# Kernel tuning notes

Hardware: AMD Instinct MI355X
Metric: run time of the kernel (lower is better)

## Reference

```python
import jax, jax.numpy as jnp
import numpy as np

DEPTH = 4  # 2**DEPTH - 1 = 15 decision nodes, 2**DEPTH = 16 leaves


def setup_inputs() -> dict:
    key = jax.random.key(0)
    k1, k2, k3, k4, k5 = jax.random.split(key, 5)
    B, S, H = 2, 2048, 1024
    n_dec, n_leaf = 2 ** DEPTH - 1, 2 ** DEPTH
    s = 1.0 / np.sqrt(H)
    return {
        "x": jax.random.normal(k1, (B, S, H), dtype=jnp.float32),
        "Wd": jax.random.normal(k2, (n_dec, H, 2), dtype=jnp.float32) * s,
        "bd": jax.random.normal(k3, (n_dec, 2), dtype=jnp.float32) * s,
        "Wl": jax.random.normal(k4, (n_leaf, H, H), dtype=jnp.float32) * s,
        "bl": jax.random.normal(k5, (n_leaf, H), dtype=jnp.float32) * s,
    }


def reference(x, Wd, bd, Wl, bl):
    B, S, H = x.shape
    # All decision nodes in one grouped GEMM: [B,S,n_dec,2], independent sigmoids
    decisions = jax.nn.sigmoid(jnp.einsum('bsh,nhk->bsnk', x, Wd) + bd)
    # Cumulative path probabilities with torch-faithful cat([p*left, p*right]) ordering
    path = jnp.ones((B, S, 1), dtype=x.dtype)
    for level in range(DEPTH):
        start = 2 ** level - 1
        lv = decisions[:, :, start:start + 2 ** level, :]  # [B,S,2^level,2]
        path = jnp.concatenate([path * lv[..., 0], path * lv[..., 1]], axis=-1)
    # Weighted leaf-output sum without materializing [B,S,n_leaf,H]
    out = jnp.einsum('bsh,lhd,bsl->bsd', x, Wl, path, optimize=True)
    out = out + jnp.einsum('bsl,ld->bsd', path, bl)
    return out
```

## Files before the change

### kernel.cpp

```cpp
#include <hip/hip_runtime.h>
#include <hip/hip_bf16.h>

typedef unsigned short u16;
typedef unsigned int u32;
typedef short bf16x8 __attribute__((ext_vector_type(8)));
typedef _Float16 f16x8 __attribute__((ext_vector_type(8)));
typedef float f32x4 __attribute__((ext_vector_type(4)));

__device__ __forceinline__ u16 f2bf(float f) {
    u32 u = __builtin_bit_cast(u32, f);
    u32 r = (u + 0x7FFFu + ((u >> 16) & 1u)) >> 16;
    return (u16)r;
}
__device__ __forceinline__ u16 f2h(float f) {
    _Float16 h = (_Float16)f;
    return __builtin_bit_cast(u16, h);
}

__device__ __forceinline__ void lds16(const void* g, void* s) {
    __builtin_amdgcn_global_load_lds(
        (const __attribute__((address_space(1))) u32*)g,
        (__attribute__((address_space(3))) u32*)s, 16, 0, 0);
}

__global__ __launch_bounds__(256) void pre_kernel(
    const float* __restrict__ x, const float* __restrict__ Wd,
    const float* __restrict__ bd, const float* __restrict__ Wl,
    float* __restrict__ path, u16* __restrict__ xb, u16* __restrict__ wlt,
    int as_f16, int M) {
    __shared__ float tile[64][65];
    const int bid = blockIdx.x;

    if (bid < 4096) {
        int nb = bid & 15, hb = (bid >> 4) & 15, l = bid >> 8;
        int t = threadIdx.x;
        int r = t >> 2, cq = (t & 3) << 4;

        const float* src = Wl + ((size_t)(l * 1024 + hb * 64 + r)) * 1024 + nb * 64 + cq;
#pragma unroll
        for (int j = 0; j < 4; ++j) {
            float4 w = ((const float4*)src)[j];
            tile[r][cq + 4 * j + 0] = w.x;
            tile[r][cq + 4 * j + 1] = w.y;
            tile[r][cq + 4 * j + 2] = w.z;
            tile[r][cq + 4 * j + 3] = w.w;
        }
        __syncthreads();
        union { u16 u[16]; uint4 q[2]; } pk;
#pragma unroll
        for (int j = 0; j < 16; ++j)
            pk.u[j] = as_f16 ? f2h(tile[cq + j][r]) : f2bf(tile[cq + j][r]);
        u16* dst = wlt + ((size_t)(l * 1024 + nb * 64 + r)) * 1024 + hb * 64 + cq;
        ((uint4*)dst)[0] = pk.q[0];
        ((uint4*)dst)[1] = pk.q[1];
        return;
    }

    int lane = threadIdx.x & 63;
    int wid = threadIdx.x >> 6;
    int m = (bid - 4096) * 4 + wid;
    if (m >= M) return;

    const float* xr = x + (size_t)m * 1024;
    float v[16];
#pragma unroll
    for (int i = 0; i < 16; ++i) v[i] = xr[lane + 64 * i];
#pragma unroll
    for (int i = 0; i < 16; ++i)
        xb[(size_t)m * 1024 + lane + 64 * i] = as_f16 ? f2h(v[i]) : f2bf(v[i]);

    int leaf = lane & 15;
    int nd[4], bit[4];
#pragma unroll
    for (int k = 0; k < 4; ++k) {
        nd[k] = (1 << k) - 1 + (leaf & ((1 << k) - 1));
        bit[k] = (leaf >> k) & 1;
    }
    float z[4] = {0.f, 0.f, 0.f, 0.f};

    const float2* Wd2 = (const float2*)Wd;
    for (int n = 0; n < 15; ++n) {
        float s0 = 0.f, s1 = 0.f;
#pragma unroll
        for (int i = 0; i < 16; ++i) {
            float2 w = Wd2[n * 1024 + lane + 64 * i];
            s0 += v[i] * w.x;
            s1 += v[i] * w.y;
        }
#pragma unroll
        for (int off = 32; off; off >>= 1) {
            s0 += __shfl_xor(s0, off, 64);
            s1 += __shfl_xor(s1, off, 64);
        }
#pragma unroll
        for (int k = 0; k < 4; ++k)
            if (nd[k] == n) z[k] = bit[k] ? s1 : s0;
    }
    float p = 1.f;
#pragma unroll
    for (int k = 0; k < 4; ++k) {
        float zz = z[k] + bd[nd[k] * 2 + bit[k]];
        p *= 1.f / (1.f + expf(-zz));
    }
    if (lane < 16) path[(size_t)m * 16 + leaf] = p;
}

__global__ __launch_bounds__(512, 2) void tree_gemm8(
    const u16* __restrict__ xh, const u16* __restrict__ wlt,
    const float* __restrict__ path, float* __restrict__ out,
    float* __restrict__ part, int M) {
    __shared__ __align__(16) u16 Asm[2][2][128 * 64];
    __shared__ __align__(16) u16 Bsm[2][2][128 * 64];
    __shared__ u16 psm_h[4][256];

    const int tid = threadIdx.x, lane = tid & 63, w = tid >> 6;
    const int wm = w >> 2, wn = w & 3;
    const int nbm = M >> 8;
    int xb_, yb_, zb_;
    {
        int bid = blockIdx.x;
        if ((nbm << 4) == 256) {
            int k = bid & 7, s = bid >> 3;
            zb_ = k >> 1; yb_ = (k & 1) * 8 + (s >> 2); xb_ = s & 3;
        } else {
            xb_ = bid & 3; int t2 = bid >> 2; yb_ = t2 % nbm; zb_ = t2 / nbm;
        }
    }
    const int n0 = xb_ * 256, m0 = yb_ * 256, z = zb_;
    const int z4 = z * 4;
    const int rl = lane >> 3;
    const int srcswz = ((lane & 7) ^ rl) << 4;
    const int arow = (lane & 15) * 128;
    const int coff0 = ((lane >> 4) << 4) ^ ((lane & 7) << 4);

    for (int i = tid; i < 1024; i += 512) {
        int r = i >> 2, lz = i & 3;
        psm_h[lz][r] = f2h(path[(size_t)(m0 + r) * 16 + z4 + lz]);
    }

#define ISSUE_A_H(dst_, ks_, h_)                                                    \
    {                                                                               \
        _Pragma("unroll") for (int j_ = 0; j_ < 2; ++j_)                            \
            lds16((const char*)xh +                                                 \
                      (size_t)(m0 + (h_) * 128 + w * 16 + j_ * 8 + rl) * 2048 +     \
                      ((ks_) << 7) + srcswz,                                        \
                  (dst_) + (h_) * 16384 + w * 2048 + j_ * 1024);                    \
    }
#define ISSUE_A(dst_, ks_) { ISSUE_A_H(dst_, ks_, 0); ISSUE_A_H(dst_, ks_, 1); }
#define ISSUE_B(dst_, t_)                                                           \
    if ((t_) < 64) {                                                                \
        size_t lb_ = (size_t)(z4 + ((t_) & 3)) * 2097152 +                          \
                     ((size_t)((t_) >> 2) << 7);                                    \
        _Pragma("unroll") for (int h_ = 0; h_ < 2; ++h_)                            \
        _Pragma("unroll") for (int j_ = 0; j_ < 2; ++j_)                            \
            lds16((const char*)wlt + lb_ +                                          \
                      (size_t)(n0 + h_ * 128 + w * 16 + j_ * 8 + rl) * 2048 +       \
                      srcswz,                                                       \
                  (dst_) + h_ * 16384 + w * 2048 + j_ * 1024);                      \
    }
#define LDA4(aB_, mfb)                                                              \
    _Pragma("unroll") for (int q_ = 0; q_ < 4; ++q_) {                              \
        aR[q_][0] = *(const f16x8*)((aB_) + ((mfb) + q_) * 2048 + coff0);           \
        aR[q_][1] = *(const f16x8*)((aB_) + ((mfb) + q_) * 2048 + (coff0 ^ 64));    \
    }
#define LDB2(bB_, nfb, d0)                                                          \
    _Pragma("unroll") for (int q_ = 0; q_ < 2; ++q_) {                              \
        bR[(d0) + q_][0] = *(const f16x8*)((bB_) + ((nfb) + q_) * 2048 + coff0);    \
        bR[(d0) + q_][1] =                                                          \
            *(const f16x8*)((bB_) + ((nfb) + q_) * 2048 + (coff0 ^ 64));            \
    }
#define LDP(ll, mfb)                                                                \
    _Pragma("unroll") for (int q_ = 0; q_ < 4; ++q_)                                \
        p2[q_] = __builtin_bit_cast(                                                \
            _Float16, psm_h[ll][wm * 128 + ((mfb) + q_) * 16 + (lane & 15)]);
#define SCALE                                                                       \
    _Pragma("unroll") for (int q_ = 0; q_ < 4; ++q_) {                              \
        aR[q_][0] *= p2[q_];                                                        \
        aR[q_][1] *= p2[q_];                                                        \
    }
#define MM(a0, b0)                                                                  \
    _Pragma("unroll") for (int mq_ = 0; mq_ < 4; ++mq_)                             \
    _Pragma("unroll") for (int nq_ = 0; nq_ < 2; ++nq_) {                           \
        acc[(a0) + mq_][(b0) + nq_] = __builtin_amdgcn_mfma_f32_16x16x32_f16(       \
            aR[mq_][0], bR[(b0) + nq_][0], acc[(a0) + mq_][(b0) + nq_], 0, 0, 0);   \
        acc[(a0) + mq_][(b0) + nq_] = __builtin_amdgcn_mfma_f32_16x16x32_f16(       \
            aR[mq_][1], bR[(b0) + nq_][1], acc[(a0) + mq_][(b0) + nq_], 0, 0, 0);   \
    }
#define BAR __builtin_amdgcn_s_barrier()
#define LG0 asm volatile("s_waitcnt lgkmcnt(0)" ::: "memory")
#define PRIO1 __builtin_amdgcn_s_setprio(1)
#define PRIO0 __builtin_amdgcn_s_setprio(0)
#define VM0 asm volatile("s_waitcnt vmcnt(0)" ::: "memory")
#define VM8 asm volatile("s_waitcnt vmcnt(8)" ::: "memory")
#define VM16 asm volatile("s_waitcnt vmcnt(16)" ::: "memory")
#define NOPX ((void)0)

#define TILE(aB_, bB_, ll, EB2, EA0, EA1, WT)                                       \
    {                                                                               \
        f16x8 aR[4][2], bR[4][2];                                                   \
        _Float16 p2[4];                                                             \
                                                                      \
        LDA4(aB_, 0); LDB2(bB_, 0, 0); LDP(ll, 0);                                  \
        BAR; LG0; SCALE; PRIO1; MM(0, 0); PRIO0; BAR;                               \
                                                                      \
        LDB2(bB_, 2, 2);                                                            \
        BAR; LG0; PRIO1; MM(0, 2); PRIO0; BAR;                                      \
                  \
        LDA4(aB_, 4); LDP(ll, 4); EB2; EA0;                                         \
        BAR; LG0; SCALE; PRIO1; MM(4, 0); PRIO0; BAR;                               \
                      \
        EA1;                                                                        \
        PRIO1; MM(4, 2); PRIO0; WT; BAR;                                            \
    }

    f32x4 acc[8][4];
#pragma unroll
    for (int a = 0; a < 8; ++a)
#pragma unroll
        for (int b = 0; b < 4; ++b) acc[a][b] = (f32x4){0.f, 0.f, 0.f, 0.f};

    const char* aBase0 = (const char*)Asm[0][wm] + arow;
    const char* aBase1 = (const char*)Asm[1][wm] + arow;
    const char* bBase0 = (const char*)Bsm[0][wn >> 1] + (wn & 1) * 8192 + arow;
    const char* bBase1 = (const char*)Bsm[1][wn >> 1] + (wn & 1) * 8192 + arow;
    char* aSlot0 = (char*)Asm[0][0];
    char* aSlot1 = (char*)Asm[1][0];
    char* bSlot0 = (char*)Bsm[0][0];
    char* bSlot1 = (char*)Bsm[1][0];

    ISSUE_A(aSlot0, 0);
    ISSUE_B(bSlot0, 0);
    ISSUE_B(bSlot1, 1);
    asm volatile("s_waitcnt vmcnt(8) lgkmcnt(0)" ::: "memory");
    BAR;
    __builtin_amdgcn_sched_barrier(0);

#pragma unroll 1
    for (int ks = 0; ks < 15; ++ks) {
        const int t4 = ks << 2;
        const char* aB = (ks & 1) ? aBase1 : aBase0;
        char* aD = (ks & 1) ? aSlot0 : aSlot1;
        TILE(aB, bBase0, 0, ISSUE_B(bSlot0, t4 + 2), NOPX, NOPX, VM8);
        TILE(aB, bBase1, 1, ISSUE_B(bSlot1, t4 + 3),
             ISSUE_A_H(aD, ks + 1, 0), ISSUE_A_H(aD, ks + 1, 1), VM16);
        TILE(aB, bBase0, 2, ISSUE_B(bSlot0, t4 + 4), NOPX, NOPX, VM16);
        TILE(aB, bBase1, 3, ISSUE_B(bSlot1, t4 + 5), NOPX, NOPX, VM8);
    }
    {
        const char* aB = aBase1;
        TILE(aB, bBase0, 0, ISSUE_B(bSlot0, 62), NOPX, NOPX, VM8);
        TILE(aB, bBase1, 1, ISSUE_B(bSlot1, 63), NOPX, NOPX, VM8);
        TILE(aB, bBase0, 2, NOPX, NOPX, NOPX, VM0);
        TILE(aB, bBase1, 3, NOPX, NOPX, NOPX, NOPX);
    }

    float* po = (z == 0) ? out : part + (size_t)(z - 1) * M * 1024;
    const int r0 = m0 + wm * 128 + ((lane >> 4) << 2);
    const int c0 = n0 + wn * 64 + (lane & 15);
#pragma unroll
    for (int mf = 0; mf < 8; ++mf)
#pragma unroll
        for (int jj = 0; jj < 4; ++jj)
#pragma unroll
            for (int nf = 0; nf < 4; ++nf)
                po[(size_t)(r0 + mf * 16 + jj) * 1024 + c0 + nf * 16] = acc[mf][nf][jj];
#undef ISSUE_A_H
#undef ISSUE_A
#undef ISSUE_B
#undef LDA4
#undef LDB2
#undef LDP
#undef SCALE
#undef MM
#undef BAR
#undef LG0
#undef PRIO1
#undef PRIO0
#undef VM0
#undef VM8
#undef VM16
#undef NOPX
#undef TILE
}

__global__ __launch_bounds__(256) void tree_gemm_fb(
    const u16* __restrict__ xb, const u16* __restrict__ wlt,
    const float* __restrict__ path, float* __restrict__ pout,
    int M, int LPB, int lgLPB) {
    __shared__ __align__(16) u16 Asm[128 * 64];
    __shared__ __align__(16) u16 Bsm[128 * 64];
    __shared__ float psm[128][16];

    const int tid = threadIdx.x, lane = tid & 63, wid = tid >> 6;
    const int wm = wid >> 1, wn = wid & 1;
    const int m0 = blockIdx.y * 128, n0 = blockIdx.x * 128;
    const int lbase = blockIdx.z * LPB;

    for (int i = tid; i < (128 << lgLPB); i += 256) {
        int r = i >> lgLPB, c = i & (LPB - 1);
        psm[r][c] = path[(size_t)(m0 + r) * 16 + lbase + c];
    }

    const int colb = (((lane & 7) ^ (lane >> 3)) << 4);
    const int rl = lane >> 3;

    f32x4 accF[4][4], accL[4][4];
#pragma unroll
    for (int a = 0; a < 4; ++a)
#pragma unroll
        for (int b = 0; b < 4; ++b) {
            accF[a][b] = (f32x4){0.f, 0.f, 0.f, 0.f};
            accL[a][b] = (f32x4){0.f, 0.f, 0.f, 0.f};
        }

    const int nsteps = LPB << 4;
    for (int sl = 0; sl < nsteps; ++sl) {
        const int l_ = lbase + (sl >> 4);
        const int h2_ = (sl & 15) << 7;
#pragma unroll
        for (int i_ = 0; i_ < 4; ++i_) {
            int seg_ = wid * 4 + i_;
            int r_ = seg_ * 8 + rl;
            lds16((const char*)xb + (size_t)(m0 + r_) * 2048 + h2_ + colb,
                  (char*)Asm + seg_ * 1024);
            lds16((const char*)wlt + (size_t)(l_ * 1024 + n0 + r_) * 2048 + h2_ + colb,
                  (char*)Bsm + seg_ * 1024);
        }
        __syncthreads();

#pragma unroll
        for (int kf = 0; kf < 2; ++kf) {
            int c2 = kf * 64 + ((lane >> 4) << 4);
            bf16x8 af[4], bfr[4];
#pragma unroll
            for (int mf = 0; mf < 4; ++mf) {
                int rr = wm * 64 + mf * 16 + (lane & 15);
                af[mf] = *(const bf16x8*)((const char*)Asm + rr * 128 + (c2 ^ ((lane & 7) << 4)));
            }
#pragma unroll
            for (int nf = 0; nf < 4; ++nf) {
                int rr = wn * 64 + nf * 16 + (lane & 15);
                bfr[nf] = *(const bf16x8*)((const char*)Bsm + rr * 128 + (c2 ^ ((lane & 7) << 4)));
            }
#pragma unroll
            for (int mf = 0; mf < 4; ++mf)
#pragma unroll
                for (int nf = 0; nf < 4; ++nf)
                    accL[mf][nf] = __builtin_amdgcn_mfma_f32_16x16x32_bf16(
                        af[mf], bfr[nf], accL[mf][nf], 0, 0, 0);
        }
        __syncthreads();

        if ((sl & 15) == 15) {
            int ll = sl >> 4;
#pragma unroll
            for (int mf = 0; mf < 4; ++mf)
#pragma unroll
                for (int jj = 0; jj < 4; ++jj) {
                    float p = psm[wm * 64 + mf * 16 + ((lane >> 4) << 2) + jj][ll];
#pragma unroll
                    for (int nf = 0; nf < 4; ++nf) {
                        accF[mf][nf][jj] += p * accL[mf][nf][jj];
                        accL[mf][nf][jj] = 0.f;
                    }
                }
        }
    }

    float* po = pout + (size_t)blockIdx.z * M * 1024;
#pragma unroll
    for (int mf = 0; mf < 4; ++mf)
#pragma unroll
        for (int jj = 0; jj < 4; ++jj) {
            int rowl = wm * 64 + mf * 16 + ((lane >> 4) << 2) + jj;
#pragma unroll
            for (int nf = 0; nf < 4; ++nf) {
                int col = n0 + wn * 64 + nf * 16 + (lane & 15);
                po[(size_t)(m0 + rowl) * 1024 + col] = accF[mf][nf][jj];
            }
        }
}

__global__ __launch_bounds__(256) void reduce_kernel(
    const float* __restrict__ extra, const float* __restrict__ path,
    const float* __restrict__ bl, float* __restrict__ out, int M,
    int nExtra, int readOut) {
    int m = blockIdx.x, t = threadIdx.x;
    size_t i4 = (size_t)m * 256 + t;
    f32x4 acc = {0.f, 0.f, 0.f, 0.f};
    if (readOut) acc = ((const f32x4*)out)[i4];
    for (int g = 0; g < nExtra; ++g)
        acc += ((const f32x4*)extra)[(size_t)g * M * 256 + i4];
#pragma unroll
    for (int l = 0; l < 16; ++l) {
        float p = path[(size_t)m * 16 + l];
        f32x4 b = ((const f32x4*)bl)[l * 256 + t];
        acc += p * b;
    }
    ((f32x4*)out)[i4] = acc;
}

extern "C" void kernel_launch(void* const* d_in, const int* in_sizes, int n_in,
                              void* d_out, int out_size, void* d_ws, size_t ws_size,
                              hipStream_t stream) {
    const float* x  = (const float*)d_in[0];
    const float* Wd = (const float*)d_in[1];
    const float* bd = (const float*)d_in[2];
    const float* Wl = (const float*)d_in[3];
    const float* bl = (const float*)d_in[4];
    float* out = (float*)d_out;

    const int H = 1024;
    const int M = in_sizes[0] / H;
    char* ws = (char*)d_ws;

    size_t n_off_xh   = (size_t)M * 16 * 4;
    size_t n_off_wlt  = n_off_xh + (size_t)M * 1024 * 2;
    size_t n_off_part = n_off_wlt + (size_t)16 * 1024 * 1024 * 2;
    size_t n_need     = n_off_part + 3 * (size_t)M * 1024 * 4;

    if (ws_size >= n_need && (M % 256) == 0) {
        float* path = (float*)ws;
        u16* xh  = (u16*)(ws + n_off_xh);
        u16* wlt = (u16*)(ws + n_off_wlt);
        float* part = (float*)(ws + n_off_part);

        pre_kernel<<<4096 + M / 4, 256, 0, stream>>>(x, Wd, bd, Wl, path, xh, wlt, 1, M);
        tree_gemm8<<<4 * (M / 256) * 4, 512, 0, stream>>>(xh, wlt, path, out, part, M);
        reduce_kernel<<<M, 256, 0, stream>>>(part, path, bl, out, M, 3, 1);
        return;
    }

    size_t off_xb   = (size_t)M * 16 * 4;
    size_t off_wlt  = off_xb + (size_t)M * 1024 * 2;
    size_t off_part = off_wlt + (size_t)16 * 1024 * 1024 * 2;
    size_t per_part = (size_t)M * 1024 * 4;

    int G = 1;
    if (ws_size >= off_part + 4 * per_part) G = 4;
    else if (ws_size >= off_part + 2 * per_part) G = 2;
    const int LPB = 16 / G;
    const int lgLPB = (G == 1) ? 4 : (G == 2) ? 3 : 2;

    float* path = (float*)ws;
    u16* xb  = (u16*)(ws + off_xb);
    u16* wlt = (u16*)(ws + off_wlt);
    float* pout = (G == 1) ? out : (float*)(ws + off_part);

    pre_kernel<<<4096 + (M + 3) / 4, 256, 0, stream>>>(x, Wd, bd, Wl, path, xb, wlt, 0, M);
    tree_gemm_fb<<<dim3(8, M / 128, G), 256, 0, stream>>>(xb, wlt, path, pout, M, LPB, lgLPB);
    reduce_kernel<<<M, 256, 0, stream>>>(pout, path, bl, out, M,
                                         (G == 1) ? 0 : G, (G == 1) ? 1 : 0);
}
```

Before: 209.1 us.

## Hold A tile in registers across leaves and triple-buffer B in LDS

The kernel now loads the full 128-row A fragment for each k-step into registers once and reuses it for all four leaves, instead of re-reading A from LDS for every leaf. A uses a single LDS buffer that is refilled mid-iteration. B gets a rotating triple buffer so prefetch runs one stage further ahead. The path scaling is fused into the MFMA loop. This cuts LDS read traffic and barriers but raises VGPR pressure through the aU[8][2] array. The A refill also relies on the new wait counts being correct.

```diff
diff --git a/kernel.cpp b/kernel.cpp
--- a/kernel.cpp
+++ b/kernel.cpp
@@ -109,8 +109,8 @@
     const u16* __restrict__ xh, const u16* __restrict__ wlt,
     const float* __restrict__ path, float* __restrict__ out,
     float* __restrict__ part, int M) {
-    __shared__ __align__(16) u16 Asm[2][2][128 * 64];
-    __shared__ __align__(16) u16 Bsm[2][2][128 * 64];
+    __shared__ __align__(16) u16 Asm[2][128 * 64];
+    __shared__ __align__(16) u16 Bsm[3][2][128 * 64];
     __shared__ u16 psm_h[4][256];
 
     const int tid = threadIdx.x, lane = tid & 63, w = tid >> 6;
@@ -138,15 +138,14 @@
         psm_h[lz][r] = f2h(path[(size_t)(m0 + r) * 16 + z4 + lz]);
     }
 
-#define ISSUE_A_H(dst_, ks_, h_)                                                    \
+#define ISSUE_A_H(ks_, h_)                                                          \
     {                                                                               \
         _Pragma("unroll") for (int j_ = 0; j_ < 2; ++j_)                            \
             lds16((const char*)xh +                                                 \
                       (size_t)(m0 + (h_) * 128 + w * 16 + j_ * 8 + rl) * 2048 +     \
                       ((ks_) << 7) + srcswz,                                        \
-                  (dst_) + (h_) * 16384 + w * 2048 + j_ * 1024);                    \
-    }
-#define ISSUE_A(dst_, ks_) { ISSUE_A_H(dst_, ks_, 0); ISSUE_A_H(dst_, ks_, 1); }
+                  (char*)Asm[0] + (h_) * 16384 + w * 2048 + j_ * 1024);             \
+    }
 #define ISSUE_B(dst_, t_)                                                           \
     if ((t_) < 64) {                                                                \
         size_t lb_ = (size_t)(z4 + ((t_) & 3)) * 2097152 +                          \
@@ -158,59 +157,65 @@
                       srcswz,                                                       \
                   (dst_) + h_ * 16384 + w * 2048 + j_ * 1024);                      \
     }
-#define LDA4(aB_, mfb)                                                              \
-    _Pragma("unroll") for (int q_ = 0; q_ < 4; ++q_) {                              \
-        aR[q_][0] = *(const f16x8*)((aB_) + ((mfb) + q_) * 2048 + coff0);           \
-        aR[q_][1] = *(const f16x8*)((aB_) + ((mfb) + q_) * 2048 + (coff0 ^ 64));    \
-    }
-#define LDB2(bB_, nfb, d0)                                                          \
+#define LDA16                                                                       \
+    _Pragma("unroll") for (int r_ = 0; r_ < 8; ++r_) {                              \
+        aU[r_][0] = *(const f16x8*)(aRd + r_ * 2048 + coff0);                       \
+        aU[r_][1] = *(const f16x8*)(aRd + r_ * 2048 + (coff0 ^ 64));                \
+    }
+#define LDB2P(b0_)                                                                  \
     _Pragma("unroll") for (int q_ = 0; q_ < 2; ++q_) {                              \
-        bR[(d0) + q_][0] = *(const f16x8*)((bB_) + ((nfb) + q_) * 2048 + coff0);    \
-        bR[(d0) + q_][1] =                                                          \
-            *(const f16x8*)((bB_) + ((nfb) + q_) * 2048 + (coff0 ^ 64));            \
-    }
-#define LDP(ll, mfb)                                                                \
-    _Pragma("unroll") for (int q_ = 0; q_ < 4; ++q_)                                \
-        p2[q_] = __builtin_bit_cast(                                                \
-            _Float16, psm_h[ll][wm * 128 + ((mfb) + q_) * 16 + (lane & 15)]);
-#define SCALE                                                                       \
-    _Pragma("unroll") for (int q_ = 0; q_ < 4; ++q_) {                              \
-        aR[q_][0] *= p2[q_];                                                        \
-        aR[q_][1] *= p2[q_];                                                        \
-    }
-#define MM(a0, b0)                                                                  \
-    _Pragma("unroll") for (int mq_ = 0; mq_ < 4; ++mq_)                             \
-    _Pragma("unroll") for (int nq_ = 0; nq_ < 2; ++nq_) {                           \
-        acc[(a0) + mq_][(b0) + nq_] = __builtin_amdgcn_mfma_f32_16x16x32_f16(       \
-            aR[mq_][0], bR[(b0) + nq_][0], acc[(a0) + mq_][(b0) + nq_], 0, 0, 0);   \
-        acc[(a0) + mq_][(b0) + nq_] = __builtin_amdgcn_mfma_f32_16x16x32_f16(       \
-            aR[mq_][1], bR[(b0) + nq_][1], acc[(a0) + mq_][(b0) + nq_], 0, 0, 0);   \
+        bR[q_][0] = *(const f16x8*)(bRdA + ((b0_) + q_) * 2048 + coff0);            \
+        bR[q_][1] = *(const f16x8*)(bRdA + ((b0_) + q_) * 2048 + (coff0 ^ 64));     \
+    }
+#define LDP8(ll)                                                                    \
+    _Pragma("unroll") for (int r_ = 0; r_ < 8; ++r_)                                \
+        pc[r_] = __builtin_bit_cast(                                                \
+            _Float16, psm_h[ll][wm * 128 + r_ * 16 + (lane & 15)]);
+#define QMM(b0_)                                                                    \
+    _Pragma("unroll") for (int r_ = 0; r_ < 8; ++r_) {                              \
+        f16x8 s0_ = aU[r_][0] * pc[r_];                                             \
+        f16x8 s1_ = aU[r_][1] * pc[r_];                                             \
+        acc[r_][(b0_)] = __builtin_amdgcn_mfma_f32_16x16x32_f16(                    \
+            s0_, bR[0][0], acc[r_][(b0_)], 0, 0, 0);                                \
+        acc[r_][(b0_)] = __builtin_amdgcn_mfma_f32_16x16x32_f16(                    \
+            s1_, bR[0][1], acc[r_][(b0_)], 0, 0, 0);                                \
+        acc[r_][(b0_) + 1] = __builtin_amdgcn_mfma_f32_16x16x32_f16(                \
+            s0_, bR[1][0], acc[r_][(b0_) + 1], 0, 0, 0);                            \
+        acc[r_][(b0_) + 1] = __builtin_amdgcn_mfma_f32_16x16x32_f16(                \
+            s1_, bR[1][1], acc[r_][(b0_) + 1], 0, 0, 0);                            \
     }
 #define BAR __builtin_amdgcn_s_barrier()
 #define LG0 asm volatile("s_waitcnt lgkmcnt(0)" ::: "memory")
 #define PRIO1 __builtin_amdgcn_s_setprio(1)
 #define PRIO0 __builtin_amdgcn_s_setprio(0)
 #define VM0 asm volatile("s_waitcnt vmcnt(0)" ::: "memory")
-#define VM8 asm volatile("s_waitcnt vmcnt(8)" ::: "memory")
-#define VM16 asm volatile("s_waitcnt vmcnt(16)" ::: "memory")
+#define VM4 asm volatile("s_waitcnt vmcnt(4)" ::: "memory")
+#define VM12 asm volatile("s_waitcnt vmcnt(12)" ::: "memory")
 #define NOPX ((void)0)
-
-#define TILE(aB_, bB_, ll, EB2, EA0, EA1, WT)                                       \
+#define ROT                                                                         \
     {                                                                               \
-        f16x8 aR[4][2], bR[4][2];                                                   \
-        _Float16 p2[4];                                                             \
-                                                                      \
-        LDA4(aB_, 0); LDB2(bB_, 0, 0); LDP(ll, 0);                                  \
-        BAR; LG0; SCALE; PRIO1; MM(0, 0); PRIO0; BAR;                               \
-                                                                      \
-        LDB2(bB_, 2, 2);                                                            \
-        BAR; LG0; PRIO1; MM(0, 2); PRIO0; BAR;                                      \
-                  \
-        LDA4(aB_, 4); LDP(ll, 4); EB2; EA0;                                         \
-        BAR; LG0; SCALE; PRIO1; MM(4, 0); PRIO0; BAR;                               \
-                      \
+        const char* tr_ = bRdA; bRdA = bRdB; bRdB = bRdC; bRdC = tr_;               \
+        char* tw_ = bWrA; bWrA = bWrB; bWrB = bWrC; bWrC = tw_;                     \
+    }
+
+#define TILE(ll, LA, EB, EA0, EA1, WT)                                              \
+    {                                                                               \
+        f16x8 bR[2][2];                                                             \
+        _Float16 pc[8];                                                             \
+                                                                 \
+        EB; EA0;                                                                    \
+        LA;                                                                         \
+        LDB2P(0);                                                                   \
+        LDP8(ll);                                                                   \
+        BAR; LG0;                                                                   \
+        PRIO1; QMM(0); PRIO0;                                                       \
+        BAR;                                                                        \
+                                                                 \
+        LDB2P(2);                                                                   \
         EA1;                                                                        \
-        PRIO1; MM(4, 2); PRIO0; WT; BAR;                                            \
+        BAR; LG0;                                                                   \
+        PRIO1; QMM(2); PRIO0;                                                       \
+        WT; BAR;                                                                    \
     }
 
     f32x4 acc[8][4];
@@ -218,40 +223,38 @@
     for (int a = 0; a < 8; ++a)
 #pragma unroll
         for (int b = 0; b < 4; ++b) acc[a][b] = (f32x4){0.f, 0.f, 0.f, 0.f};
-
-    const char* aBase0 = (const char*)Asm[0][wm] + arow;
-    const char* aBase1 = (const char*)Asm[1][wm] + arow;
-    const char* bBase0 = (const char*)Bsm[0][wn >> 1] + (wn & 1) * 8192 + arow;
-    const char* bBase1 = (const char*)Bsm[1][wn >> 1] + (wn & 1) * 8192 + arow;
-    char* aSlot0 = (char*)Asm[0][0];
-    char* aSlot1 = (char*)Asm[1][0];
-    char* bSlot0 = (char*)Bsm[0][0];
-    char* bSlot1 = (char*)Bsm[1][0];
-
-    ISSUE_A(aSlot0, 0);
-    ISSUE_B(bSlot0, 0);
-    ISSUE_B(bSlot1, 1);
-    asm volatile("s_waitcnt vmcnt(8) lgkmcnt(0)" ::: "memory");
+    f16x8 aU[8][2];
+
+    const char* aRd = (const char*)Asm[wm] + arow;
+    const int bOff = (wn >> 1) * 16384 + (wn & 1) * 8192 + arow;
+    const char* bRdA = (const char*)Bsm[0][0] + bOff;
+    const char* bRdB = (const char*)Bsm[1][0] + bOff;
+    const char* bRdC = (const char*)Bsm[2][0] + bOff;
+    char* bWrA = (char*)Bsm[0][0];
+    char* bWrB = (char*)Bsm[1][0];
+    char* bWrC = (char*)Bsm[2][0];
+
+    ISSUE_A_H(0, 0); ISSUE_A_H(0, 1);
+    ISSUE_B(bWrA, 0);
+    ISSUE_B(bWrB, 1);
+    asm volatile("s_waitcnt vmcnt(4) lgkmcnt(0)" ::: "memory");
     BAR;
     __builtin_amdgcn_sched_barrier(0);
 
 #pragma unroll 1
     for (int ks = 0; ks < 15; ++ks) {
         const int t4 = ks << 2;
-        const char* aB = (ks & 1) ? aBase1 : aBase0;
-        char* aD = (ks & 1) ? aSlot0 : aSlot1;
-        TILE(aB, bBase0, 0, ISSUE_B(bSlot0, t4 + 2), NOPX, NOPX, VM8);
-        TILE(aB, bBase1, 1, ISSUE_B(bSlot1, t4 + 3),
-             ISSUE_A_H(aD, ks + 1, 0), ISSUE_A_H(aD, ks + 1, 1), VM16);
-        TILE(aB, bBase0, 2, ISSUE_B(bSlot0, t4 + 4), NOPX, NOPX, VM16);
-        TILE(aB, bBase1, 3, ISSUE_B(bSlot1, t4 + 5), NOPX, NOPX, VM8);
+        TILE(0, LDA16, ISSUE_B(bWrC, t4 + 2), NOPX, NOPX, VM4); ROT;
+        TILE(1, NOPX, ISSUE_B(bWrC, t4 + 3), NOPX, NOPX, VM4); ROT;
+        TILE(2, NOPX, ISSUE_B(bWrC, t4 + 4),
+             ISSUE_A_H(ks + 1, 0), ISSUE_A_H(ks + 1, 1), VM12); ROT;
+        TILE(3, NOPX, ISSUE_B(bWrC, t4 + 5), NOPX, NOPX, VM4); ROT;
     }
     {
-        const char* aB = aBase1;
-        TILE(aB, bBase0, 0, ISSUE_B(bSlot0, 62), NOPX, NOPX, VM8);
-        TILE(aB, bBase1, 1, ISSUE_B(bSlot1, 63), NOPX, NOPX, VM8);
-        TILE(aB, bBase0, 2, NOPX, NOPX, NOPX, VM0);
-        TILE(aB, bBase1, 3, NOPX, NOPX, NOPX, NOPX);
+        TILE(0, LDA16, ISSUE_B(bWrC, 62), NOPX, NOPX, VM4); ROT;
+        TILE(1, NOPX, ISSUE_B(bWrC, 63), NOPX, NOPX, VM4); ROT;
+        TILE(2, NOPX, NOPX, NOPX, NOPX, VM0); ROT;
+        TILE(3, NOPX, NOPX, NOPX, NOPX, NOPX);
     }
 
     float* po = (z == 0) ? out : part + (size_t)(z - 1) * M * 1024;
@@ -265,21 +268,20 @@
             for (int nf = 0; nf < 4; ++nf)
                 po[(size_t)(r0 + mf * 16 + jj) * 1024 + c0 + nf * 16] = acc[mf][nf][jj];
 #undef ISSUE_A_H
-#undef ISSUE_A
 #undef ISSUE_B
-#undef LDA4
-#undef LDB2
-#undef LDP
-#undef SCALE
-#undef MM
+#undef LDA16
+#undef LDB2P
+#undef LDP8
+#undef QMM
 #undef BAR
 #undef LG0
 #undef PRIO1
 #undef PRIO0
 #undef VM0
-#undef VM8
-#undef VM16
+#undef VM4
+#undef VM12
 #undef NOPX
+#undef ROT
 #undef TILE
 }
 
```

Measured after the change: 546.6 us. 2.61x slower.

## Split prologue into path and weight-transpose kernels; merge MFMA phases per tile

Applied to the files above, without the earlier changes.

The combined preprocessing kernel becomes two launches: one computes path probabilities and converts x, the other transposes and converts Wl. Inside the main GEMM each tile now loads both B halves together and runs MFMA in two larger phases instead of four, which removes two barrier pairs per tile. The vmcnt wait thresholds are adjusted to fit the new issue order. This cuts synchronisation overhead but adds an extra kernel launch, raises LDS-read register pressure, and changes how load latency is hidden. The fallback path also drops the round-up in its path-kernel grid size, so it now assumes M is a multiple of 4.

```diff
diff --git a/kernel.cpp b/kernel.cpp
--- a/kernel.cpp
+++ b/kernel.cpp
@@ -23,42 +23,13 @@
         (__attribute__((address_space(3))) u32*)s, 16, 0, 0);
 }
 
-__global__ __launch_bounds__(256) void pre_kernel(
+__global__ __launch_bounds__(256) void path_kernel(
     const float* __restrict__ x, const float* __restrict__ Wd,
-    const float* __restrict__ bd, const float* __restrict__ Wl,
-    float* __restrict__ path, u16* __restrict__ xb, u16* __restrict__ wlt,
-    int as_f16, int M) {
-    __shared__ float tile[64][65];
-    const int bid = blockIdx.x;
-
-    if (bid < 4096) {
-        int nb = bid & 15, hb = (bid >> 4) & 15, l = bid >> 8;
-        int t = threadIdx.x;
-        int r = t >> 2, cq = (t & 3) << 4;
-
-        const float* src = Wl + ((size_t)(l * 1024 + hb * 64 + r)) * 1024 + nb * 64 + cq;
-#pragma unroll
-        for (int j = 0; j < 4; ++j) {
-            float4 w = ((const float4*)src)[j];
-            tile[r][cq + 4 * j + 0] = w.x;
-            tile[r][cq + 4 * j + 1] = w.y;
-            tile[r][cq + 4 * j + 2] = w.z;
-            tile[r][cq + 4 * j + 3] = w.w;
-        }
-        __syncthreads();
-        union { u16 u[16]; uint4 q[2]; } pk;
-#pragma unroll
-        for (int j = 0; j < 16; ++j)
-            pk.u[j] = as_f16 ? f2h(tile[cq + j][r]) : f2bf(tile[cq + j][r]);
-        u16* dst = wlt + ((size_t)(l * 1024 + nb * 64 + r)) * 1024 + hb * 64 + cq;
-        ((uint4*)dst)[0] = pk.q[0];
-        ((uint4*)dst)[1] = pk.q[1];
-        return;
-    }
-
+    const float* __restrict__ bd, float* __restrict__ path,
+    u16* __restrict__ xb, int as_f16, int M) {
     int lane = threadIdx.x & 63;
     int wid = threadIdx.x >> 6;
-    int m = (bid - 4096) * 4 + wid;
+    int m = blockIdx.x * 4 + wid;
     if (m >= M) return;
 
     const float* xr = x + (size_t)m * 1024;
@@ -103,6 +74,32 @@
         p *= 1.f / (1.f + expf(-zz));
     }
     if (lane < 16) path[(size_t)m * 16 + leaf] = p;
+}
+
+__global__ __launch_bounds__(256) void wlt_kernel(
+    const float* __restrict__ Wl, u16* __restrict__ wlt, int as_f16) {
+    __shared__ float tile[64][65];
+    int l = blockIdx.z, hb = blockIdx.y, nb = blockIdx.x;
+    int t = threadIdx.x;
+    int r = t >> 2, cq = (t & 3) << 4;
+
+    const float* src = Wl + ((size_t)(l * 1024 + hb * 64 + r)) * 1024 + nb * 64 + cq;
+#pragma unroll
+    for (int j = 0; j < 4; ++j) {
+        float4 w = ((const float4*)src)[j];
+        tile[r][cq + 4 * j + 0] = w.x;
+        tile[r][cq + 4 * j + 1] = w.y;
+        tile[r][cq + 4 * j + 2] = w.z;
+        tile[r][cq + 4 * j + 3] = w.w;
+    }
+    __syncthreads();
+    union { u16 u[16]; uint4 q[2]; } pk;
+#pragma unroll
+    for (int j = 0; j < 16; ++j)
+        pk.u[j] = as_f16 ? f2h(tile[cq + j][r]) : f2bf(tile[cq + j][r]);
+    u16* dst = wlt + ((size_t)(l * 1024 + nb * 64 + r)) * 1024 + hb * 64 + cq;
+    ((uint4*)dst)[0] = pk.q[0];
+    ((uint4*)dst)[1] = pk.q[1];
 }
 
 __global__ __launch_bounds__(512, 2) void tree_gemm8(
@@ -192,25 +189,21 @@
 #define PRIO0 __builtin_amdgcn_s_setprio(0)
 #define VM0 asm volatile("s_waitcnt vmcnt(0)" ::: "memory")
 #define VM8 asm volatile("s_waitcnt vmcnt(8)" ::: "memory")
-#define VM16 asm volatile("s_waitcnt vmcnt(16)" ::: "memory")
+#define VM12 asm volatile("s_waitcnt vmcnt(12)" ::: "memory")
 #define NOPX ((void)0)
 
 #define TILE(aB_, bB_, ll, EB2, EA0, EA1, WT)                                       \
     {                                                                               \
         f16x8 aR[4][2], bR[4][2];                                                   \
         _Float16 p2[4];                                                             \
-                                                                      \
-        LDA4(aB_, 0); LDB2(bB_, 0, 0); LDP(ll, 0);                                  \
-        BAR; LG0; SCALE; PRIO1; MM(0, 0); PRIO0; BAR;                               \
-                                                                      \
-        LDB2(bB_, 2, 2);                                                            \
-        BAR; LG0; PRIO1; MM(0, 2); PRIO0; BAR;                                      \
-                  \
-        LDA4(aB_, 4); LDP(ll, 4); EB2; EA0;                                         \
-        BAR; LG0; SCALE; PRIO1; MM(4, 0); PRIO0; BAR;                               \
-                      \
-        EA1;                                                                        \
-        PRIO1; MM(4, 2); PRIO0; WT; BAR;                                            \
+                                                      \
+        LDA4(aB_, 0); LDB2(bB_, 0, 0); LDB2(bB_, 2, 2); LDP(ll, 0);                 \
+        BAR; LG0; SCALE;                                                            \
+        PRIO1; MM(0, 0); MM(0, 2); PRIO0; BAR;                                      \
+                                  \
+        LDA4(aB_, 4); LDP(ll, 4); EB2; EA0; EA1;                                    \
+        BAR; LG0; SCALE;                                                            \
+        PRIO1; MM(4, 0); MM(4, 2); PRIO0; WT; BAR;                                  \
     }
 
     f32x4 acc[8][4];
@@ -242,8 +235,8 @@
         char* aD = (ks & 1) ? aSlot0 : aSlot1;
         TILE(aB, bBase0, 0, ISSUE_B(bSlot0, t4 + 2), NOPX, NOPX, VM8);
         TILE(aB, bBase1, 1, ISSUE_B(bSlot1, t4 + 3),
-             ISSUE_A_H(aD, ks + 1, 0), ISSUE_A_H(aD, ks + 1, 1), VM16);
-        TILE(aB, bBase0, 2, ISSUE_B(bSlot0, t4 + 4), NOPX, NOPX, VM16);
+             ISSUE_A_H(aD, ks + 1, 0), ISSUE_A_H(aD, ks + 1, 1), VM12);
+        TILE(aB, bBase0, 2, ISSUE_B(bSlot0, t4 + 4), NOPX, NOPX, VM8);
         TILE(aB, bBase1, 3, ISSUE_B(bSlot1, t4 + 5), NOPX, NOPX, VM8);
     }
     {
@@ -278,7 +271,7 @@
 #undef PRIO0
 #undef VM0
 #undef VM8
-#undef VM16
+#undef VM12
 #undef NOPX
 #undef TILE
 }
@@ -425,7 +418,8 @@
         u16* wlt = (u16*)(ws + n_off_wlt);
         float* part = (float*)(ws + n_off_part);
 
-        pre_kernel<<<4096 + M / 4, 256, 0, stream>>>(x, Wd, bd, Wl, path, xh, wlt, 1, M);
+        path_kernel<<<M / 4, 256, 0, stream>>>(x, Wd, bd, path, xh, 1, M);
+        wlt_kernel<<<dim3(16, 16, 16), 256, 0, stream>>>(Wl, wlt, 1);
         tree_gemm8<<<4 * (M / 256) * 4, 512, 0, stream>>>(xh, wlt, path, out, part, M);
         reduce_kernel<<<M, 256, 0, stream>>>(part, path, bl, out, M, 3, 1);
         return;
@@ -447,7 +441,8 @@
     u16* wlt = (u16*)(ws + off_wlt);
     float* pout = (G == 1) ? out : (float*)(ws + off_part);
 
-    pre_kernel<<<4096 + (M + 3) / 4, 256, 0, stream>>>(x, Wd, bd, Wl, path, xb, wlt, 0, M);
+    path_kernel<<<M / 4, 256, 0, stream>>>(x, Wd, bd, path, xb, 0, M);
+    wlt_kernel<<<dim3(16, 16, 16), 256, 0, stream>>>(Wl, wlt, 0);
     tree_gemm_fb<<<dim3(8, M / 128, G), 256, 0, stream>>>(xb, wlt, path, pout, M, LPB, lgLPB);
     reduce_kernel<<<M, 256, 0, stream>>>(pout, path, bl, out, M,
                                          (G == 1) ? 0 : G, (G == 1) ? 1 : 0);
```

Result: faster. 202.0 us (-3.4%).
